# Performance work log

Measured on AMD Instinct MI355X. Metric: run time of the kernel, lower is better.

The kernel has to match this reference:

```python
import jax, jax.numpy as jnp
import numpy as np

B, S, D_MODEL, N_HEADS, D_K, D_V = 32, 512, 256, 16, 16, 16


def setup_inputs() -> dict:
    key = jax.random.key(0)
    ks = jax.random.split(key, 9)
    def xavier(k, fan_in, fan_out):
        lim = np.sqrt(6.0 / (fan_in + fan_out)).astype(np.float32)
        return jax.random.uniform(k, (fan_out, fan_in), jnp.float32, -lim, lim)
    return {
        "Q": jax.random.normal(ks[0], (B, S, D_MODEL), jnp.float32),
        "K": jax.random.normal(ks[1], (B, S, D_MODEL), jnp.float32),
        "V": jax.random.normal(ks[2], (B, S, D_MODEL), jnp.float32),
        "mask": jnp.ones((B, S), jnp.float32),
        "W_Q": xavier(ks[3], D_MODEL, N_HEADS * D_K),
        "b_Q": jnp.zeros((N_HEADS * D_K,), jnp.float32),
        "W_K": xavier(ks[4], D_MODEL, N_HEADS * D_K),
        "b_K": jnp.zeros((N_HEADS * D_K,), jnp.float32),
        "W_V": xavier(ks[5], D_MODEL, N_HEADS * D_V),
        "b_V": jnp.zeros((N_HEADS * D_V,), jnp.float32),
    }


def reference(Q, K, V, mask, W_Q, b_Q, W_K, b_K, W_V, b_V):
    # Projections: torch Linear stores weight as (out, in) -> x @ W.T + b
    def proj(x, W, b, d):
        y = jnp.einsum('bsd,ed->bse', x, W) + b  # [B,S,H*d]
        return y.reshape(B, S, N_HEADS, d).transpose(0, 2, 1, 3)  # [B,H,S,d]
    q = proj(Q, W_Q, b_Q, D_K)
    k = proj(K, W_K, b_K, D_K)
    v = proj(V, W_V, b_V, D_V)
    # Unstabilized exp-score attention with multiplicative mask
    scores = jnp.exp(jnp.einsum('bhqd,bhkd->bhqk', q, k) / np.sqrt(D_K).astype(np.float32))
    scores = scores * mask[:, None, None, :]  # mask over key axis
    attn = scores / (jnp.sum(scores, axis=-1, keepdims=True) + 1e-8)
    ctx = jnp.einsum('bhqk,bhkd->bhqd', attn, v)  # [B,H,S,D_V]
    return ctx.transpose(0, 2, 1, 3).reshape(B, S, N_HEADS * D_V)
```

## Files before the change

kernel.cpp:

```cpp
#include <hip/hip_runtime.h>
#include <hip/hip_bf16.h>


#define PROJ_ELEMS (32 * 16 * 512 * 16)
#define LOG2E 1.44269504088896f

typedef _Float16 f16x4 __attribute__((ext_vector_type(4)));
typedef float    f32x4 __attribute__((ext_vector_type(4)));

static __device__ __forceinline__ f16x4 cvt4(float4 v) {
    f16x4 r;
    r[0] = (_Float16)v.x; r[1] = (_Float16)v.y;
    r[2] = (_Float16)v.z; r[3] = (_Float16)v.w;
    return r;
}

__global__ __launch_bounds__(256, 2) void proj_mfma(
    const float* __restrict__ Qx, const float* __restrict__ Kx, const float* __restrict__ Vx,
    const float* __restrict__ WQ, const float* __restrict__ bQ,
    const float* __restrict__ WK, const float* __restrict__ bK,
    const float* __restrict__ WV, const float* __restrict__ bV,
    _Float16* __restrict__ qh, _Float16* __restrict__ kh, _Float16* __restrict__ vth)
{
    const int proj = blockIdx.z;
    const float* __restrict__ X  = (proj == 0) ? Qx : (proj == 1) ? Kx : Vx;
    const float* __restrict__ W  = (proj == 0) ? WQ : (proj == 1) ? WK : WV;
    const float* __restrict__ bb = (proj == 0) ? bQ : (proj == 1) ? bK : bV;

    const int row0 = blockIdx.x * 64;
    const int t = threadIdx.x;
    const int w = t >> 6, l = t & 63;
    const int lm16 = l & 15, lg = l >> 4;

    const float* xbase[4];
    const float* wbase[4];
#pragma unroll
    for (int mi = 0; mi < 4; mi++)
        xbase[mi] = X + (size_t)(row0 + mi * 16 + lm16) * 256 + lg * 4;
#pragma unroll
    for (int ni = 0; ni < 4; ni++)
        wbase[ni] = W + (size_t)(w * 64 + ni * 16 + lm16) * 256 + lg * 4;

    f32x4 acc[4][4];
#pragma unroll
    for (int mi = 0; mi < 4; mi++)
#pragma unroll
        for (int ni = 0; ni < 4; ni++) acc[mi][ni] = (f32x4){0.f, 0.f, 0.f, 0.f};

#pragma unroll 1
    for (int k0 = 0; k0 < 256; k0 += 64) {
        float4 xr[4][4], wr[4][4];
#pragma unroll
        for (int kq = 0; kq < 4; kq++) {
#pragma unroll
            for (int mi = 0; mi < 4; mi++)
                xr[kq][mi] = *(const float4*)(xbase[mi] + k0 + kq * 16);
#pragma unroll
            for (int ni = 0; ni < 4; ni++)
                wr[kq][ni] = *(const float4*)(wbase[ni] + k0 + kq * 16);
        }
#pragma unroll
        for (int kq = 0; kq < 4; kq++) {
            f16x4 xf[4], wf[4];
#pragma unroll
            for (int mi = 0; mi < 4; mi++) xf[mi] = cvt4(xr[kq][mi]);
#pragma unroll
            for (int ni = 0; ni < 4; ni++) wf[ni] = cvt4(wr[kq][ni]);

            if (proj < 2) {
#pragma unroll
                for (int mi = 0; mi < 4; mi++)
#pragma unroll
                    for (int ni = 0; ni < 4; ni++)
                        acc[mi][ni] = __builtin_amdgcn_mfma_f32_16x16x16f16(
                            wf[ni], xf[mi], acc[mi][ni], 0, 0, 0);
            } else {
#pragma unroll
                for (int mi = 0; mi < 4; mi++)
#pragma unroll
                    for (int ni = 0; ni < 4; ni++)
                        acc[mi][ni] = __builtin_amdgcn_mfma_f32_16x16x16f16(
                            xf[mi], wf[ni], acc[mi][ni], 0, 0, 0);
            }
        }
    }

    const int bq = row0 >> 9;
    const int sbase = row0 & 511;

    if (proj < 2) {
        const float scl = (proj == 0) ? 0.25f * LOG2E : 1.0f;
        _Float16* __restrict__ outp = (proj == 0) ? qh : kh;
#pragma unroll
        for (int mi = 0; mi < 4; mi++) {
            const int s = sbase + mi * 16 + lm16;
#pragma unroll
            for (int ni = 0; ni < 4; ni++) {
                const int col0 = w * 64 + ni * 16 + lg * 4;
                const int h = col0 >> 4, d0 = col0 & 15;
                const float4 bv = *(const float4*)&bb[col0];
                _Float16 tmp[4];
                tmp[0] = (_Float16)((acc[mi][ni][0] + bv.x) * scl);
                tmp[1] = (_Float16)((acc[mi][ni][1] + bv.y) * scl);
                tmp[2] = (_Float16)((acc[mi][ni][2] + bv.z) * scl);
                tmp[3] = (_Float16)((acc[mi][ni][3] + bv.w) * scl);
                *(f16x4*)&outp[(((size_t)bq * 16 + h) * 512 + s) * 16 + d0] =
                    *(const f16x4*)tmp;
            }
        }
    } else {
#pragma unroll
        for (int mi = 0; mi < 4; mi++) {
            const int s0 = sbase + mi * 16 + lg * 4;
#pragma unroll
            for (int ni = 0; ni < 4; ni++) {
                const int col = w * 64 + ni * 16 + lm16;
                const int h = col >> 4, d = col & 15;
                const float bc = bb[col];
                _Float16 tmp[4];
#pragma unroll
                for (int r = 0; r < 4; r++)
                    tmp[r] = (_Float16)(acc[mi][ni][r] + bc);
                *(f16x4*)&vth[(((size_t)bq * 16 + h) * 16 + d) * 512 + s0] =
                    *(const f16x4*)tmp;
            }
        }
    }
}

__global__ __launch_bounds__(256, 4) void attn_mfma(
    const _Float16* __restrict__ qh, const _Float16* __restrict__ kh,
    const _Float16* __restrict__ vth, const float* __restrict__ mask,
    float* __restrict__ out)
{
    const int blk  = blockIdx.x;
    const int bh   = blk >> 1;
    const int half = blk & 1;
    const int b = bh >> 4, h = bh & 15;

    __shared__ _Float16 ks[512 * 16];
    __shared__ _Float16 vt[16 * 528];
    __shared__ float    lm[512];
    __shared__ float    sums[256];

    const int t = threadIdx.x;
    const int w = t >> 6, l = t & 63;
    const int lm16 = l & 15, lg = l >> 4;

    {
        const float4* src = (const float4*)(kh + (size_t)bh * 8192);
        float4* dst = (float4*)ks;
#pragma unroll
        for (int i = 0; i < 4; i++) dst[t + i * 256] = src[t + i * 256];
    }
    {
        const _Float16* src = vth + (size_t)bh * 8192;
#pragma unroll
        for (int i = 0; i < 4; i++) {
            int f = t + i * 256;
            int d = f >> 6, c = f & 63;
            *(float4*)&vt[d * 528 + c * 8] = *(const float4*)&src[d * 512 + c * 8];
        }
    }
    {
#pragma unroll
        for (int i = 0; i < 2; i++) {
            int j = t + i * 256;
            lm[j] = __builtin_amdgcn_logf(mask[b * 512 + j]);
        }
    }

    f16x4 qf[4];
    {
        const _Float16* qb = qh + (size_t)bh * 8192;
#pragma unroll
        for (int mt = 0; mt < 4; mt++) {
            int m = half * 256 + w * 64 + mt * 16 + lm16;
            qf[mt] = *(const f16x4*)&qb[m * 16 + lg * 4];
        }
    }

    f32x4 acc[4];
    float rs[4];
#pragma unroll
    for (int mt = 0; mt < 4; mt++) {
        acc[mt] = (f32x4){0.f, 0.f, 0.f, 0.f};
        rs[mt] = 0.f;
    }

    __syncthreads();

    for (int jt = 0; jt < 32; jt++) {
        const int j0 = jt << 4;
        f16x4 ka = *(const f16x4*)&ks[(j0 + lm16) * 16 + lg * 4];
        f16x4 vb = *(const f16x4*)&vt[lm16 * 528 + j0 + lg * 4];
        f32x4 lmv = *(const f32x4*)&lm[j0 + lg * 4];
#pragma unroll
        for (int mt = 0; mt < 4; mt++) {
            f32x4 s4 = __builtin_amdgcn_mfma_f32_16x16x16f16(ka, qf[mt], lmv, 0, 0, 0);
            float e0 = __builtin_amdgcn_exp2f(s4[0]);
            float e1 = __builtin_amdgcn_exp2f(s4[1]);
            float e2 = __builtin_amdgcn_exp2f(s4[2]);
            float e3 = __builtin_amdgcn_exp2f(s4[3]);
            rs[mt] += (e0 + e1) + (e2 + e3);
            f16x4 pa;
            pa[0] = (_Float16)e0; pa[1] = (_Float16)e1;
            pa[2] = (_Float16)e2; pa[3] = (_Float16)e3;
            acc[mt] = __builtin_amdgcn_mfma_f32_16x16x16f16(pa, vb, acc[mt], 0, 0, 0);
        }
    }

#pragma unroll
    for (int mt = 0; mt < 4; mt++) {
        float r = rs[mt];
        r += __shfl_xor(r, 16);
        r += __shfl_xor(r, 32);
        if (l < 16) sums[w * 64 + mt * 16 + l] = r;
    }
    __syncthreads();

#pragma unroll
    for (int mt = 0; mt < 4; mt++) {
        f32x4 sv = *(const f32x4*)&sums[w * 64 + mt * 16 + lg * 4];
        int m = half * 256 + w * 64 + mt * 16 + lg * 4;
        float* o = out + ((size_t)(b * 512 + m) * 256) + h * 16 + lm16;
        o[0]   = acc[mt][0] / (sv[0] + 1e-8f);
        o[256] = acc[mt][1] / (sv[1] + 1e-8f);
        o[512] = acc[mt][2] / (sv[2] + 1e-8f);
        o[768] = acc[mt][3] / (sv[3] + 1e-8f);
    }
}

extern "C" void kernel_launch(void* const* d_in, const int* in_sizes, int n_in,
                              void* d_out, int out_size, void* d_ws, size_t ws_size,
                              hipStream_t stream) {
    const float* Q    = (const float*)d_in[0];
    const float* K    = (const float*)d_in[1];
    const float* V    = (const float*)d_in[2];
    const float* mask = (const float*)d_in[3];
    const float* W_Q  = (const float*)d_in[4];
    const float* b_Q  = (const float*)d_in[5];
    const float* W_K  = (const float*)d_in[6];
    const float* b_K  = (const float*)d_in[7];
    const float* W_V  = (const float*)d_in[8];
    const float* b_V  = (const float*)d_in[9];
    float* out = (float*)d_out;

    _Float16* qh  = (_Float16*)d_ws;
    _Float16* kh  = qh + PROJ_ELEMS;
    _Float16* vth = kh + PROJ_ELEMS;

    proj_mfma<<<dim3(256, 1, 3), 256, 0, stream>>>(
        Q, K, V, W_Q, b_Q, W_K, b_K, W_V, b_V, qh, kh, vth);

    attn_mfma<<<dim3(32 * 16 * 2), 256, 0, stream>>>(qh, kh, vth, mask, out);
}
```

Baseline: 180.6 us.

## Stage projection tiles through double-buffered swizzled LDS via direct global-to-LDS loads

The projection kernel now loads X and W tiles straight into LDS with global_load_lds, double-buffered across the K loop, instead of each wave loading its own fp32 fragments into registers. The block tile becomes 128 rows by 128 columns, with column blocks spread over gridDim.y, so waves share the staged data and global reads of W are no longer repeated per wave. An XOR swizzle is applied to avoid LDS bank conflicts. In exchange the kernel uses 64KB of LDS per block, which limits occupancy, and adds barriers on every K step.

```diff
diff --git a/kernel.cpp b/kernel.cpp
--- a/kernel.cpp
+++ b/kernel.cpp
@@ -13,6 +13,13 @@
     r[0] = (_Float16)v.x; r[1] = (_Float16)v.y;
     r[2] = (_Float16)v.z; r[3] = (_Float16)v.w;
     return r;
+}
+
+static __device__ __forceinline__ void gl_lds16(const void* g, void* l) {
+    __builtin_amdgcn_global_load_lds(
+        (const __attribute__((address_space(1))) unsigned int*)g,
+        (__attribute__((address_space(3))) unsigned int*)l,
+        16, 0, 0);
 }
 
 __global__ __launch_bounds__(256, 2) void proj_mfma(
@@ -27,46 +34,59 @@
     const float* __restrict__ W  = (proj == 0) ? WQ : (proj == 1) ? WK : WV;
     const float* __restrict__ bb = (proj == 0) ? bQ : (proj == 1) ? bK : bV;
 
-    const int row0 = blockIdx.x * 64;
+    const int row0 = blockIdx.x * 128;
+    const int colb = blockIdx.y;
     const int t = threadIdx.x;
     const int w = t >> 6, l = t & 63;
     const int lm16 = l & 15, lg = l >> 4;
 
-    const float* xbase[4];
-    const float* wbase[4];
+    __shared__ float4 lds4[4096];
+    char* ldsc = (char*)lds4;
+
+    const int rw = w * 32 + (l >> 3);
+    const int swzs = ((l & 7) * 16) ^ ((rw & 7) << 4);
+    const char* gx = (const char*)X + (size_t)(row0 + rw) * 1024 + swzs;
+    const char* gw = (const char*)W + (size_t)(colb * 128 + rw) * 1024 + swzs;
+
+#define STAGE(buf, ks) do {                                                  \
+    char* bx_ = ldsc + (buf) * 32768;                                        \
+    char* bw_ = bx_ + 16384;                                                 \
+    _Pragma("unroll")                                                        \
+    for (int j = 0; j < 4; j++) {                                            \
+        gl_lds16(gx + (ks) * 128 + j * 8192, bx_ + w * 4096 + j * 1024);     \
+        gl_lds16(gw + (ks) * 128 + j * 8192, bw_ + w * 4096 + j * 1024);     \
+    } } while (0)
+
+    f32x4 acc[4][4];
 #pragma unroll
     for (int mi = 0; mi < 4; mi++)
-        xbase[mi] = X + (size_t)(row0 + mi * 16 + lm16) * 256 + lg * 4;
-#pragma unroll
-    for (int ni = 0; ni < 4; ni++)
-        wbase[ni] = W + (size_t)(w * 64 + ni * 16 + lm16) * 256 + lg * 4;
-
-    f32x4 acc[4][4];
-#pragma unroll
-    for (int mi = 0; mi < 4; mi++)
 #pragma unroll
         for (int ni = 0; ni < 4; ni++) acc[mi][ni] = (f32x4){0.f, 0.f, 0.f, 0.f};
 
+    const int fswz = (lm16 & 7) << 4;
+
+    STAGE(0, 0);
+    __syncthreads();
+
 #pragma unroll 1
-    for (int k0 = 0; k0 < 256; k0 += 64) {
-        float4 xr[4][4], wr[4][4];
-#pragma unroll
-        for (int kq = 0; kq < 4; kq++) {
-#pragma unroll
-            for (int mi = 0; mi < 4; mi++)
-                xr[kq][mi] = *(const float4*)(xbase[mi] + k0 + kq * 16);
-#pragma unroll
-            for (int ni = 0; ni < 4; ni++)
-                wr[kq][ni] = *(const float4*)(wbase[ni] + k0 + kq * 16);
-        }
-#pragma unroll
-        for (int kq = 0; kq < 4; kq++) {
+    for (int ks = 0; ks < 8; ks++) {
+        if (ks < 7) STAGE((ks + 1) & 1, ks + 1);
+        const char* xt = ldsc + (ks & 1) * 32768;
+        const char* wt = xt + 16384;
+#pragma unroll
+        for (int s = 0; s < 2; s++) {
+            const int inrow = (s * 64 + lg * 16) ^ fswz;
             f16x4 xf[4], wf[4];
 #pragma unroll
-            for (int mi = 0; mi < 4; mi++) xf[mi] = cvt4(xr[kq][mi]);
-#pragma unroll
-            for (int ni = 0; ni < 4; ni++) wf[ni] = cvt4(wr[kq][ni]);
-
+            for (int mi = 0; mi < 4; mi++) {
+                const int row = (w & 1) * 64 + mi * 16 + lm16;
+                xf[mi] = cvt4(*(const float4*)(xt + row * 128 + inrow));
+            }
+#pragma unroll
+            for (int ni = 0; ni < 4; ni++) {
+                const int row = (w >> 1) * 64 + ni * 16 + lm16;
+                wf[ni] = cvt4(*(const float4*)(wt + row * 128 + inrow));
+            }
             if (proj < 2) {
 #pragma unroll
                 for (int mi = 0; mi < 4; mi++)
@@ -83,7 +103,9 @@
                             xf[mi], wf[ni], acc[mi][ni], 0, 0, 0);
             }
         }
-    }
+        __syncthreads();
+    }
+#undef STAGE
 
     const int bq = row0 >> 9;
     const int sbase = row0 & 511;
@@ -93,10 +115,10 @@
         _Float16* __restrict__ outp = (proj == 0) ? qh : kh;
 #pragma unroll
         for (int mi = 0; mi < 4; mi++) {
-            const int s = sbase + mi * 16 + lm16;
+            const int s = sbase + (w & 1) * 64 + mi * 16 + lm16;
 #pragma unroll
             for (int ni = 0; ni < 4; ni++) {
-                const int col0 = w * 64 + ni * 16 + lg * 4;
+                const int col0 = colb * 128 + (w >> 1) * 64 + ni * 16 + lg * 4;
                 const int h = col0 >> 4, d0 = col0 & 15;
                 const float4 bv = *(const float4*)&bb[col0];
                 _Float16 tmp[4];
@@ -111,10 +133,10 @@
     } else {
 #pragma unroll
         for (int mi = 0; mi < 4; mi++) {
-            const int s0 = sbase + mi * 16 + lg * 4;
+            const int s0 = sbase + (w & 1) * 64 + mi * 16 + lg * 4;
 #pragma unroll
             for (int ni = 0; ni < 4; ni++) {
-                const int col = w * 64 + ni * 16 + lm16;
+                const int col = colb * 128 + (w >> 1) * 64 + ni * 16 + lm16;
                 const int h = col >> 4, d = col & 15;
                 const float bc = bb[col];
                 _Float16 tmp[4];
@@ -250,7 +272,7 @@
     _Float16* kh  = qh + PROJ_ELEMS;
     _Float16* vth = kh + PROJ_ELEMS;
 
-    proj_mfma<<<dim3(256, 1, 3), 256, 0, stream>>>(
+    proj_mfma<<<dim3(128, 2, 3), 256, 0, stream>>>(
         Q, K, V, W_Q, b_Q, W_K, b_K, W_V, b_V, qh, kh, vth);
 
     attn_mfma<<<dim3(32 * 16 * 2), 256, 0, stream>>>(qh, kh, vth, mask, out);
```

Result: faster. 152.9 us (-15.3%).
